# Kernel optimization log

Hardware: AMD Instinct MI355X
Metric: run time of the kernel (lower is better)

Reference implementation:

```python
import jax, jax.numpy as jnp
import numpy as np

EPS = 1e-08


def setup_inputs() -> dict:
    key = jax.random.key(0)
    kx, km = jax.random.split(key)
    B, T, D = 128, 4096, 64
    x = jax.random.normal(kx, (B, T, D), dtype=jnp.float32)
    mask = jax.random.randint(km, (B, T, D), 0, 2).astype(jnp.float32)
    return {"x": x, "mask": mask}


def reference(x, mask):
    B, T, D = x.shape
    dt = x.dtype

    # ---- temporal: lag-1 autocorrelation + linear trend ----
    autocorr = jnp.mean(x[:, :-1, :] * x[:, 1:, :], axis=(1, 2))[:, None]  # (B,1)
    t = jnp.arange(T, dtype=dt)
    t_c = t - t.mean()
    x_mean_t = x.mean(axis=2)                                   # (B,T)
    num = (t_c * (x_mean_t - x_mean_t.mean(axis=1, keepdims=True))).sum(axis=1, keepdims=True)
    trend = num / ((t_c ** 2).sum() + EPS)                      # (B,1)

    # ---- frequency: dominant frequency + spectral entropy ----
    power = jnp.abs(jnp.fft.rfft(x_mean_t, axis=1)) ** 2        # (B,T//2+1)
    dom_freq = (jnp.argmax(power, axis=1).astype(dt) / (T / 2))[:, None]
    p_norm = power / (power.sum(axis=1, keepdims=True) + EPS)
    spec_ent = -(p_norm * jnp.log(p_norm + EPS)).sum(axis=1, keepdims=True)

    # ---- statistical: skewness, kurtosis, quantiles ----
    xc = x - x.mean(axis=(1, 2), keepdims=True)
    m2 = (xc ** 2).mean(axis=(1, 2))
    m3 = (xc ** 3).mean(axis=(1, 2))
    m4 = (xc ** 4).mean(axis=(1, 2))
    skew = m3 / (m2 ** 1.5 + EPS)
    kurt = m4 / (m2 ** 2 + EPS)
    q = jnp.quantile(x.reshape(B, -1), jnp.array([0.25, 0.5, 0.75]), axis=1)  # (3,B)
    stat = jnp.stack([skew, kurt, q[0], q[1], q[2]], axis=1)    # (B,5)

    # ---- shape: peaks, zero crossings, rate of change ----
    diff = x_mean_t[:, 1:] - x_mean_t[:, :-1]                   # (B,T-1)
    peak = (diff[:, 1:] * diff[:, :-1] < 0).astype(dt).sum(axis=1, keepdims=True) / (T - 2)
    xmc = x_mean_t - x_mean_t.mean(axis=1, keepdims=True)
    zero_cross = (xmc[:, 1:] * xmc[:, :-1] < 0).astype(dt).sum(axis=1, keepdims=True) / (T - 1)
    roc = jnp.abs(diff).mean(axis=1, keepdims=True)

    # ---- missing-data features (vectorized, no per-batch loop) ----
    missing_rate = 1.0 - mask.reshape(B, -1).sum(axis=1, keepdims=True) / (T * D + EPS)
    obs_per_time = mask.sum(axis=2)                             # (B,T)
    obs_density = obs_per_time / (D + EPS)
    density_var = jnp.var(obs_density, axis=1, ddof=1, keepdims=True)  # unbiased, matches torch
    time_mask = obs_per_time > 0                                # (B,T) bool
    first_idx = jnp.argmax(time_mask, axis=1).astype(dt)
    first_obs = jnp.where(time_mask.any(axis=1), first_idx / T, 0.0)[:, None]

    # ---- channel features: mean off-diagonal correlation + PCA var explained ----
    xcc = x - x.mean(axis=1, keepdims=True)                     # (B,T,D)
    gram = jnp.einsum('btd,bte->bde', xcc, xcc)                 # (B,D,D)
    cov = gram / (T - 1 + EPS)
    std = jnp.std(x, axis=1, ddof=1)                            # (B,D), unbiased like torch.std
    corr = cov / (std[:, :, None] * std[:, None, :] + EPS)
    off_diag = 1.0 - jnp.eye(D, dtype=dt)
    mean_corr = ((corr * off_diag).sum(axis=(1, 2)) / (D * (D - 1) + EPS))[:, None]
    # singular values squared of xcc == eigenvalues of gram
    eig = jnp.linalg.eigvalsh(gram)                             # ascending, (B,D)
    var_explained = (eig[:, -1] / eig.sum(axis=1))[:, None]

    return jnp.concatenate([
        autocorr, trend,               # temporal (2)
        dom_freq, spec_ent,            # frequency (2)
        stat,                          # statistical (5)
        peak, zero_cross, roc,         # shape (3)
        missing_rate, density_var, first_obs,  # missing (3)
        mean_corr, var_explained,      # channel (2)
    ], axis=1)                          # (B,17)
```

## Files before the change

### kernel.cpp

```cpp
#include <hip/hip_runtime.h>
#include <math.h>

#define TB 128
#define TT 4096
#define TD 64

#define GRAM_OFF   0u
#define HIST_OFF   2097152u
#define COLSUM_OFF 4194304u
#define SCAL_OFF   4227072u
#define FIRST_OFF  4230656u
#define ZERO_BYTES 4231168u
#define XMEAN_OFF  4231168u

typedef float  f32x4  __attribute__((ext_vector_type(4)));
typedef short  s16x8  __attribute__((ext_vector_type(8)));

__device__ __forceinline__ float brs4(float v, float* sbuf, int tid) {
#pragma unroll
  for (int o = 32; o; o >>= 1) v += __shfl_xor(v, o);
  __syncthreads();
  if ((tid & 63) == 0) sbuf[tid >> 6] = v;
  __syncthreads();
  return (sbuf[0] + sbuf[1]) + (sbuf[2] + sbuf[3]);
}

__device__ __forceinline__ float brs8(float v, float* sbuf, int tid) {
#pragma unroll
  for (int o = 32; o; o >>= 1) v += __shfl_xor(v, o);
  __syncthreads();
  if ((tid & 63) == 0) sbuf[tid >> 6] = v;
  __syncthreads();
  return ((sbuf[0] + sbuf[1]) + (sbuf[2] + sbuf[3])) +
         ((sbuf[4] + sbuf[5]) + (sbuf[6] + sbuf[7]));
}

__device__ __forceinline__ int binof(float v) {
  int bi = (int)floorf(fmaf(v, 256.f, 2048.f));
  return bi < 0 ? 0 : (bi > 4095 ? 4095 : bi);
}

__device__ __forceinline__ unsigned short f2bf(float f) {
  unsigned u = __float_as_uint(f);
  return (unsigned short)((u + 0x7FFFu + ((u >> 16) & 1u)) >> 16);
}

__global__ __launch_bounds__(256) void kA_stats(const float* __restrict__ x,
    const float* __restrict__ mk, float* __restrict__ xmean,
    unsigned long long* __restrict__ hist64, float* __restrict__ colsum,
    float* __restrict__ scal, int* __restrict__ firstg) {
  __shared__ unsigned shist[4096];
  __shared__ float xrow[256];
  __shared__ float scol[64];
  __shared__ float sred[4];
  __shared__ int smax[4];

  const int tid  = threadIdx.x;
  const int b    = blockIdx.y;
  const int s    = blockIdx.x;
  const int t0   = s << 8;
  const int lane = tid & 63;
  const int wv   = tid >> 6;
  const int q    = lane >> 4;
  const int c    = lane & 15;
  const int lcol = c << 2;
  const int tw   = t0 + (wv << 6);

  for (int i = tid; i < 4096; i += 256) shist[i] = 0u;
  if (tid < 64) scol[tid] = 0.f;
  __syncthreads();

  float s1 = 0.f, s2 = 0.f, s3 = 0.f, s4 = 0.f, ac = 0.f;
  float osum = 0.f, o2 = 0.f;
  int fmax = 0;
  float cs0 = 0.f, cs1 = 0.f, cs2 = 0.f, cs3 = 0.f;
  float4 pv = make_float4(0.f, 0.f, 0.f, 0.f);

  const float* xb = x + (size_t)b * (TT * TD);
  const float* mb = mk + (size_t)b * (TT * TD);

  for (int it = 0; it < 16; ++it) {
    const int t = tw + (it << 2) + q;
    const float4 v = *(const float4*)(xb + (size_t)t * TD + lcol);
    const float4 m = *(const float4*)(mb + (size_t)t * TD + lcol);
    {
      const float x0 = v.x, x1 = v.y, x2 = v.z, x3 = v.w;
      const float q0 = x0 * x0, q1 = x1 * x1, q2 = x2 * x2, q3 = x3 * x3;
      s1 += (x0 + x1) + (x2 + x3);
      s2 += (q0 + q1) + (q2 + q3);
      s3 += (q0 * x0 + q1 * x1) + (q2 * x2 + q3 * x3);
      s4 += (q0 * q0 + q1 * q1) + (q2 * q2 + q3 * q3);
      cs0 += x0; cs1 += x1; cs2 += x2; cs3 += x3;
      atomicAdd(&shist[binof(x0)], 1u);
      atomicAdd(&shist[binof(x1)], 1u);
      atomicAdd(&shist[binof(x2)], 1u);
      atomicAdd(&shist[binof(x3)], 1u);
    }
    {
      float rx = (v.x + v.y) + (v.z + v.w);
      float rm = (m.x + m.y) + (m.z + m.w);
      rx += __shfl_xor(rx, 1); rm += __shfl_xor(rm, 1);
      rx += __shfl_xor(rx, 2); rm += __shfl_xor(rm, 2);
      rx += __shfl_xor(rx, 4); rm += __shfl_xor(rm, 4);
      rx += __shfl_xor(rx, 8); rm += __shfl_xor(rm, 8);
      if (c == 0) {
        xrow[t - t0] = rx * (1.f / 64.f);
        osum += rm;
        o2 = fmaf(rm, rm, o2);
        if (rm > 0.f) fmax = max(fmax, TT - t);
      }
    }
    {
      const float n0 = __shfl(v.x, lane + 16);
      const float n1 = __shfl(v.y, lane + 16);
      const float n2 = __shfl(v.z, lane + 16);
      const float n3 = __shfl(v.w, lane + 16);
      const float d1 = (v.x * n0 + v.y * n1) + (v.z * n2 + v.w * n3);
      ac += (q < 3) ? d1 : 0.f;
      const float b0 = __shfl(v.x, c);
      const float b1 = __shfl(v.y, c);
      const float b2 = __shfl(v.z, c);
      const float b3 = __shfl(v.w, c);
      if (it > 0) {
        const float d2 = (pv.x * b0 + pv.y * b1) + (pv.z * b2 + pv.w * b3);
        ac += (q == 3) ? d2 : 0.f;
      }
      pv = v;
    }
  }
  {
    const int tnext = tw + 64;
    if (tnext < TT) {
      const float4 nb = *(const float4*)(xb + (size_t)tnext * TD + lcol);
      const float d2 = (pv.x * nb.x + pv.y * nb.y) + (pv.z * nb.z + pv.w * nb.w);
      ac += (q == 3) ? d2 : 0.f;
    }
  }
  __syncthreads();
  xmean[(size_t)b * TT + t0 + tid] = xrow[tid];
  const float rac = brs4(ac, sred, tid);
  const float r1 = brs4(s1, sred, tid);
  const float r2 = brs4(s2, sred, tid);
  const float r3 = brs4(s3, sred, tid);
  const float r4 = brs4(s4, sred, tid);
  const float ro = brs4(osum, sred, tid);
  const float ro2 = brs4(o2, sred, tid);
#pragma unroll
  for (int o = 32; o; o >>= 1) fmax = max(fmax, __shfl_xor(fmax, o));
  if ((tid & 63) == 0) smax[tid >> 6] = fmax;
  __syncthreads();
  if (tid == 0) {
    atomicAdd(&scal[0 * TB + b], rac);
    atomicAdd(&scal[1 * TB + b], r1);
    atomicAdd(&scal[2 * TB + b], r2);
    atomicAdd(&scal[3 * TB + b], r3);
    atomicAdd(&scal[4 * TB + b], r4);
    atomicAdd(&scal[5 * TB + b], ro);
    atomicAdd(&scal[6 * TB + b], ro2);
    atomicMax(&firstg[b], max(max(smax[0], smax[1]), max(smax[2], smax[3])));
  }
  atomicAdd(&scol[lcol + 0], cs0);
  atomicAdd(&scol[lcol + 1], cs1);
  atomicAdd(&scol[lcol + 2], cs2);
  atomicAdd(&scol[lcol + 3], cs3);
  __syncthreads();
  if (tid < 64) atomicAdd(&colsum[b * 64 + tid], scol[tid]);
  unsigned long long* hb = hist64 + (size_t)b * 2048;
  const int rot = (s * 331) & 2047;
  for (int i0 = tid; i0 < 2048; i0 += 256) {
    const int i = (i0 + rot) & 2047;
    const unsigned lo = shist[2 * i];
    const unsigned hi = shist[2 * i + 1];
    if (lo | hi)
      atomicAdd(&hb[i], (unsigned long long)lo | ((unsigned long long)hi << 32));
  }
}

__global__ __launch_bounds__(256) void kB_gram(const float* __restrict__ x,
                                               float* __restrict__ gram) {
  __shared__ __align__(16) unsigned short Xt[2][64 * 72];
  const int tid  = threadIdx.x;
  const int b    = blockIdx.y;
  const int s    = blockIdx.x;
  const int t0   = s << 9;
  const int lane = tid & 63;
  const int wv   = tid >> 6;
  const int g    = tid >> 4;
  const int r0   = g << 2;
  const int c    = tid & 15;
  const int lcol = c << 2;
  const int mb0 = (wv & 1) << 5;
  const int nb0 = (wv >> 1) << 5;
  const int ml  = lane & 15;
  const int qk  = (lane >> 4) << 3;

  f32x4 acc[2][2];
#pragma unroll
  for (int mi = 0; mi < 2; ++mi)
#pragma unroll
    for (int ni = 0; ni < 2; ++ni) acc[mi][ni] = (f32x4)0.f;

  const float* xb = x + (size_t)b * (TT * TD);

  int p = 0;
  for (int tile = 0; tile < 8; ++tile) {
    const int tbase = t0 + (tile << 6);
    float4 v[4];
#pragma unroll
    for (int k = 0; k < 4; ++k)
      v[k] = *(const float4*)(xb + (size_t)(tbase + r0 + k) * TD + lcol);
#pragma unroll
    for (int j = 0; j < 4; ++j) {
      const float e0 = j == 0 ? v[0].x : (j == 1 ? v[0].y : (j == 2 ? v[0].z : v[0].w));
      const float e1 = j == 0 ? v[1].x : (j == 1 ? v[1].y : (j == 2 ? v[1].z : v[1].w));
      const float e2 = j == 0 ? v[2].x : (j == 1 ? v[2].y : (j == 2 ? v[2].z : v[2].w));
      const float e3 = j == 0 ? v[3].x : (j == 1 ? v[3].y : (j == 2 ? v[3].z : v[3].w));
      uint2 pw;
      pw.x = (unsigned)f2bf(e0) | ((unsigned)f2bf(e1) << 16);
      pw.y = (unsigned)f2bf(e2) | ((unsigned)f2bf(e3) << 16);
      *(uint2*)(&Xt[p][(lcol + j) * 72 + r0]) = pw;
    }
    __syncthreads();
#pragma unroll
    for (int kk = 0; kk < 2; ++kk) {
      const int ko = (kk << 5) + qk;
      s16x8 af[2], bf[2];
#pragma unroll
      for (int mi = 0; mi < 2; ++mi)
        af[mi] = *(const s16x8*)(&Xt[p][(mb0 + (mi << 4) + ml) * 72 + ko]);
#pragma unroll
      for (int ni = 0; ni < 2; ++ni)
        bf[ni] = *(const s16x8*)(&Xt[p][(nb0 + (ni << 4) + ml) * 72 + ko]);
#pragma unroll
      for (int mi = 0; mi < 2; ++mi)
#pragma unroll
        for (int ni = 0; ni < 2; ++ni)
          acc[mi][ni] = __builtin_amdgcn_mfma_f32_16x16x32_bf16(
              af[mi], bf[ni], acc[mi][ni], 0, 0, 0);
    }
    p ^= 1;
  }
  float* gb = gram + (size_t)b * 4096;
  const int crow = (lane >> 4) << 2;
  const int ccol = lane & 15;
#pragma unroll
  for (int mi = 0; mi < 2; ++mi)
#pragma unroll
    for (int ni = 0; ni < 2; ++ni) {
      const int gr0 = mb0 + (mi << 4) + crow;
      const int gc = nb0 + (ni << 4) + ccol;
#pragma unroll
      for (int rg = 0; rg < 4; ++rg)
        atomicAdd(&gb[(gr0 + rg) * 64 + gc], acc[mi][ni][rg]);
    }
}

__global__ __launch_bounds__(512) void k34(const float* __restrict__ xmean,
    const float* __restrict__ gram, const float* __restrict__ colsum,
    const unsigned* __restrict__ hist, const float* __restrict__ scal,
    const int* __restrict__ firstg, float* __restrict__ out) {
  __shared__ __align__(16) char arena[49152];
  __shared__ float sred[8];
  __shared__ float smv[8];
  __shared__ int smi[8];
  __shared__ float cssh[64];
  __shared__ float sdsh[64];
  __shared__ float osv_s[6];
  const int tid = threadIdx.x;

  if (blockIdx.x < 128) {
    const int b = blockIdx.x;
    float* xm = (float*)arena;
    float* re = xm + 4096;
    float* im = re + 4096;
    const float* xb = xmean + (size_t)b * TT;
    for (int i = tid; i < TT; i += 512) xm[i] = xb[i];
    __syncthreads();
    float ls = 0.f;
    for (int i = tid; i < TT; i += 512) ls += xm[i];
    const float meanv = brs8(ls, sred, tid) * (1.f / TT);
    float tnum = 0.f, roc = 0.f;
    int pk = 0, zc = 0;
    for (int i = tid; i < TT; i += 512) {
      const float xi = xm[i];
      tnum += ((float)i - 2047.5f) * (xi - meanv);
      if (i < TT - 1) {
        const float d1 = xm[i + 1] - xi;
        roc += fabsf(d1);
        if (i >= 1) {
          const float d0 = xi - xm[i - 1];
          if (d1 * d0 < 0.f) ++pk;
        }
      }
      if (i >= 1) {
        if ((xi - meanv) * (xm[i - 1] - meanv) < 0.f) ++zc;
      }
    }
    tnum = brs8(tnum, sred, tid);
    roc = brs8(roc, sred, tid);
    const float pkf = brs8((float)pk, sred, tid);
    const float zcf = brs8((float)zc, sred, tid);
    if (tid == 0) {
      out[b * 17 + 1] = tnum / 5726622720.0f;
      out[b * 17 + 9] = pkf * (1.f / 4094.f);
      out[b * 17 + 10] = zcf * (1.f / 4095.f);
      out[b * 17 + 11] = roc * (1.f / 4095.f);
    }
    for (int i = tid; i < TT; i += 512) {
      re[i] = xm[__brev((unsigned)i) >> 20];
      im[i] = 0.f;
    }
    __syncthreads();
    int l2h = 0;
    for (int len = 2; len <= TT; len <<= 1, ++l2h) {
      const int half = len >> 1;
      const float ab = -6.283185307179586f / (float)len;
      for (int j = tid; j < TT / 2; j += 512) {
        const int pos = j & (half - 1);
        const int i0 = ((j >> l2h) << (l2h + 1)) + pos;
        const int i1 = i0 + half;
        float sn, cn;
        __sincosf(ab * (float)pos, &sn, &cn);
        const float vr = re[i1], vi = im[i1];
        const float tr = cn * vr - sn * vi;
        const float ti = cn * vi + sn * vr;
        const float ur = re[i0], ui = im[i0];
        re[i0] = ur + tr; im[i0] = ui + ti;
        re[i1] = ur - tr; im[i1] = ui - ti;
      }
      __syncthreads();
    }
    float ps = 0.f, bmaxv = -1.f;
    int bidx = 0;
    for (int k = tid; k <= 2048; k += 512) {
      const float p = re[k] * re[k] + im[k] * im[k];
      ps += p;
      if (p > bmaxv) { bmaxv = p; bidx = k; }
    }
    ps = brs8(ps, sred, tid);
#pragma unroll
    for (int o = 32; o; o >>= 1) {
      const float ov = __shfl_xor(bmaxv, o);
      const int oi = __shfl_xor(bidx, o);
      if (ov > bmaxv || (ov == bmaxv && oi < bidx)) { bmaxv = ov; bidx = oi; }
    }
    if ((tid & 63) == 0) { smv[tid >> 6] = bmaxv; smi[tid >> 6] = bidx; }
    __syncthreads();
    float ent = 0.f;
    const float inv = 1.f / (ps + 1e-8f);
    for (int k = tid; k <= 2048; k += 512) {
      const float p = (re[k] * re[k] + im[k] * im[k]) * inv;
      ent -= p * __logf(p + 1e-8f);
    }
    ent = brs8(ent, sred, tid);
    if (tid == 0) {
      float bv = smv[0]; int bi = smi[0];
      for (int w = 1; w < 8; ++w)
        if (smv[w] > bv || (smv[w] == bv && smi[w] < bi)) { bv = smv[w]; bi = smi[w]; }
      out[b * 17 + 2] = (float)bi * (1.f / 2048.f);
      out[b * 17 + 3] = ent;
    }
  } else {
    const int b = blockIdx.x - 128;
    float* Lg = (float*)arena;
    unsigned* h = (unsigned*)(arena + 16640);
    unsigned* cumc = (unsigned*)(arena + 16640 + 16384);
    if (tid < 64) cssh[tid] = colsum[b * 64 + tid];
    for (int i = tid; i < 4096; i += 512) h[i] = hist[(size_t)b * 4096 + i];
    __syncthreads();
    const float* gb = gram + (size_t)b * 4096;
    for (int i = tid; i < 4096; i += 512) {
      const int d = i >> 6, e = i & 63;
      Lg[d * 65 + e] = gb[i] - cssh[d] * cssh[e] * (1.f / 4096.f);
    }
    unsigned chs_own = 0;
    if (tid < 256) {
#pragma unroll
      for (int j = 0; j < 16; ++j) chs_own += h[(tid << 4) + j];
      cumc[tid] = chs_own;
    }
    __syncthreads();
    if (tid < 64) sdsh[tid] = sqrtf(Lg[tid * 65 + tid] * (1.f / 4095.f));
    for (int off = 1; off < 256; off <<= 1) {
      unsigned add = 0;
      if (tid < 256 && tid >= off) add = cumc[tid - off];
      __syncthreads();
      if (tid < 256) cumc[tid] += add;
      __syncthreads();
    }
    float mcs = 0.f, trc = 0.f;
    for (int i = tid; i < 4096; i += 512) {
      const int d = i >> 6, e = i & 63;
      const float gv = Lg[d * 65 + e];
      if (d != e) mcs += (gv * (1.f / 4095.f)) / (sdsh[d] * sdsh[e] + 1e-8f);
      else trc += gv;
    }
    mcs = brs8(mcs, sred, tid);
    trc = brs8(trc, sred, tid);
    if (tid < 256) {
      const unsigned ranks[6] = {65535u, 65536u, 131071u, 131072u, 196607u, 196608u};
      const unsigned incl = cumc[tid];
      const unsigned excl = incl - chs_own;
#pragma unroll
      for (int qi = 0; qi < 6; ++qi) {
        const unsigned r = ranks[qi];
        if (excl <= r && r < incl) {
          int bin = tid << 4;
          unsigned cum = excl;
          while (bin < 4095 && cum + h[bin] <= r) { cum += h[bin]; ++bin; }
          const float cnt = (float)max(h[bin], 1u);
          osv_s[qi] = ((float)bin * (1.f / 256.f) - 8.f) +
                      (((float)(r - cum) + 0.5f) / cnt) * (1.f / 256.f);
        }
      }
    }
    float lam = 0.f;
    if (tid < 64) {
      const float* rowp = &Lg[tid * 65];
      float v = 1.f + 0.001f * (float)tid;
      float n2 = 1.f;
      for (int it = 0; it < 48; ++it) {
        float w0 = 0.f, w1 = 0.f, w2 = 0.f, w3 = 0.f;
#pragma unroll
        for (int e = 0; e < 64; e += 4) {
          w0 = fmaf(rowp[e],     __shfl(v, e),     w0);
          w1 = fmaf(rowp[e + 1], __shfl(v, e + 1), w1);
          w2 = fmaf(rowp[e + 2], __shfl(v, e + 2), w2);
          w3 = fmaf(rowp[e + 3], __shfl(v, e + 3), w3);
        }
        const float w = (w0 + w1) + (w2 + w3);
        n2 = w * w;
#pragma unroll
        for (int o = 32; o; o >>= 1) n2 += __shfl_xor(n2, o);
        v = w * rsqrtf(n2);
      }
      lam = sqrtf(n2);
    }
    __syncthreads();
    if (tid == 0) {
      const float q25 = 0.25f * osv_s[0] + 0.75f * osv_s[1];
      const float q50 = 0.5f * (osv_s[2] + osv_s[3]);
      const float q75 = 0.75f * osv_s[4] + 0.25f * osv_s[5];
      const float N = 262144.f;
      const float m1 = scal[1 * TB + b] / N;
      const float M2 = scal[2 * TB + b] / N;
      const float M3 = scal[3 * TB + b] / N;
      const float M4 = scal[4 * TB + b] / N;
      const float mu2 = M2 - m1 * m1;
      const float mu3 = M3 - 3.f * m1 * M2 + 2.f * m1 * m1 * m1;
      const float mu4 = M4 - 4.f * m1 * M3 + 6.f * m1 * m1 * M2 - 3.f * m1 * m1 * m1 * m1;
      const float skew = mu3 / (sqrtf(mu2) * mu2 + 1e-8f);
      const float kurt = mu4 / (mu2 * mu2 + 1e-8f);
      const float acv = scal[0 * TB + b] * (1.f / 262080.f);
      const float msum = scal[5 * TB + b];
      const float o2s = scal[6 * TB + b];
      const float missing = 1.f - msum / 262144.f;
      const float sdm = msum * (1.f / 64.f) * (1.f / 4096.f);
      const float dvar = (o2s * (1.f / 4096.f) - 4096.f * sdm * sdm) * (1.f / 4095.f);
      const int fm = firstg[b];
      const float fobs = fm > 0 ? (float)(4096 - fm) * (1.f / 4096.f) : 0.f;
      float* ob = out + b * 17;
      ob[0] = acv;
      ob[4] = skew; ob[5] = kurt;
      ob[6] = q25; ob[7] = q50; ob[8] = q75;
      ob[12] = missing; ob[13] = dvar; ob[14] = fobs;
      ob[15] = mcs / (4032.f + 1e-8f);
      ob[16] = lam / trc;
    }
  }
}

extern "C" void kernel_launch(void* const* d_in, const int* in_sizes, int n_in,
                              void* d_out, int out_size, void* d_ws, size_t ws_size,
                              hipStream_t stream) {
  (void)in_sizes; (void)n_in; (void)out_size; (void)ws_size;
  const float* x = (const float*)d_in[0];
  const float* mask = (const float*)d_in[1];
  float* out = (float*)d_out;
  char* ws = (char*)d_ws;
  float* gram = (float*)(ws + GRAM_OFF);
  unsigned* hist = (unsigned*)(ws + HIST_OFF);
  unsigned long long* hist64 = (unsigned long long*)(ws + HIST_OFF);
  float* colsum = (float*)(ws + COLSUM_OFF);
  float* scal = (float*)(ws + SCAL_OFF);
  int* firstg = (int*)(ws + FIRST_OFF);
  float* xmean = (float*)(ws + XMEAN_OFF);

  hipMemsetAsync(d_ws, 0, ZERO_BYTES, stream);

  dim3 gA(16, TB);
  kA_stats<<<gA, 256, 0, stream>>>(x, mask, xmean, hist64, colsum, scal, firstg);
  dim3 gB(8, TB);
  kB_gram<<<gB, 256, 0, stream>>>(x, gram);
  k34<<<256, 512, 0, stream>>>(xmean, gram, colsum, hist, scal, firstg, out);
}
```

Measured before the change: 358.7 us.

## Process four consecutive rows per thread in stats kernel, halve block count

```diff
diff --git a/kernel.cpp b/kernel.cpp
--- a/kernel.cpp
+++ b/kernel.cpp
@@ -50,7 +50,7 @@
     unsigned long long* __restrict__ hist64, float* __restrict__ colsum,
     float* __restrict__ scal, int* __restrict__ firstg) {
   __shared__ unsigned shist[4096];
-  __shared__ float xrow[256];
+  __shared__ float xrow[512];
   __shared__ float scol[64];
   __shared__ float sred[4];
   __shared__ int smax[4];
@@ -58,13 +58,11 @@
   const int tid  = threadIdx.x;
   const int b    = blockIdx.y;
   const int s    = blockIdx.x;
-  const int t0   = s << 8;
-  const int lane = tid & 63;
-  const int wv   = tid >> 6;
-  const int q    = lane >> 4;
-  const int c    = lane & 15;
+  const int t0   = s << 9;
+  const int g    = tid >> 4;
+  const int r0   = g << 2;
+  const int c    = tid & 15;
   const int lcol = c << 2;
-  const int tw   = t0 + (wv << 6);
 
   for (int i = tid; i < 4096; i += 256) shist[i] = 0u;
   if (tid < 64) scol[tid] = 0.f;
@@ -74,17 +72,25 @@
   float osum = 0.f, o2 = 0.f;
   int fmax = 0;
   float cs0 = 0.f, cs1 = 0.f, cs2 = 0.f, cs3 = 0.f;
-  float4 pv = make_float4(0.f, 0.f, 0.f, 0.f);
 
   const float* xb = x + (size_t)b * (TT * TD);
   const float* mb = mk + (size_t)b * (TT * TD);
 
-  for (int it = 0; it < 16; ++it) {
-    const int t = tw + (it << 2) + q;
-    const float4 v = *(const float4*)(xb + (size_t)t * TD + lcol);
-    const float4 m = *(const float4*)(mb + (size_t)t * TD + lcol);
-    {
-      const float x0 = v.x, x1 = v.y, x2 = v.z, x3 = v.w;
+  for (int tile = 0; tile < 8; ++tile) {
+    const int r = t0 + (tile << 6) + r0;
+    float4 v[4], m[4];
+#pragma unroll
+    for (int k = 0; k < 4; ++k)
+      v[k] = *(const float4*)(xb + (size_t)(r + k) * TD + lcol);
+#pragma unroll
+    for (int k = 0; k < 4; ++k)
+      m[k] = *(const float4*)(mb + (size_t)(r + k) * TD + lcol);
+    float4 nx = make_float4(0.f, 0.f, 0.f, 0.f);
+    if (r + 4 < TT)
+      nx = *(const float4*)(xb + (size_t)(r + 4) * TD + lcol);
+#pragma unroll
+    for (int k = 0; k < 4; ++k) {
+      const float x0 = v[k].x, x1 = v[k].y, x2 = v[k].z, x3 = v[k].w;
       const float q0 = x0 * x0, q1 = x1 * x1, q2 = x2 * x2, q3 = x3 * x3;
       s1 += (x0 + x1) + (x2 + x3);
       s2 += (q0 + q1) + (q2 + q3);
@@ -96,48 +102,30 @@
       atomicAdd(&shist[binof(x2)], 1u);
       atomicAdd(&shist[binof(x3)], 1u);
     }
-    {
-      float rx = (v.x + v.y) + (v.z + v.w);
-      float rm = (m.x + m.y) + (m.z + m.w);
+#pragma unroll
+    for (int k = 0; k < 4; ++k) {
+      float rx = (v[k].x + v[k].y) + (v[k].z + v[k].w);
+      float rm = (m[k].x + m[k].y) + (m[k].z + m[k].w);
       rx += __shfl_xor(rx, 1); rm += __shfl_xor(rm, 1);
       rx += __shfl_xor(rx, 2); rm += __shfl_xor(rm, 2);
       rx += __shfl_xor(rx, 4); rm += __shfl_xor(rm, 4);
       rx += __shfl_xor(rx, 8); rm += __shfl_xor(rm, 8);
       if (c == 0) {
+        const int t = r + k;
         xrow[t - t0] = rx * (1.f / 64.f);
         osum += rm;
         o2 = fmaf(rm, rm, o2);
         if (rm > 0.f) fmax = max(fmax, TT - t);
       }
     }
-    {
-      const float n0 = __shfl(v.x, lane + 16);
-      const float n1 = __shfl(v.y, lane + 16);
-      const float n2 = __shfl(v.z, lane + 16);
-      const float n3 = __shfl(v.w, lane + 16);
-      const float d1 = (v.x * n0 + v.y * n1) + (v.z * n2 + v.w * n3);
-      ac += (q < 3) ? d1 : 0.f;
-      const float b0 = __shfl(v.x, c);
-      const float b1 = __shfl(v.y, c);
-      const float b2 = __shfl(v.z, c);
-      const float b3 = __shfl(v.w, c);
-      if (it > 0) {
-        const float d2 = (pv.x * b0 + pv.y * b1) + (pv.z * b2 + pv.w * b3);
-        ac += (q == 3) ? d2 : 0.f;
-      }
-      pv = v;
-    }
+    ac += (v[0].x * v[1].x + v[0].y * v[1].y) + (v[0].z * v[1].z + v[0].w * v[1].w);
+    ac += (v[1].x * v[2].x + v[1].y * v[2].y) + (v[1].z * v[2].z + v[1].w * v[2].w);
+    ac += (v[2].x * v[3].x + v[2].y * v[3].y) + (v[2].z * v[3].z + v[2].w * v[3].w);
+    ac += (v[3].x * nx.x + v[3].y * nx.y) + (v[3].z * nx.z + v[3].w * nx.w);
   }
-  {
-    const int tnext = tw + 64;
-    if (tnext < TT) {
-      const float4 nb = *(const float4*)(xb + (size_t)tnext * TD + lcol);
-      const float d2 = (pv.x * nb.x + pv.y * nb.y) + (pv.z * nb.z + pv.w * nb.w);
-      ac += (q == 3) ? d2 : 0.f;
-    }
-  }
   __syncthreads();
   xmean[(size_t)b * TT + t0 + tid] = xrow[tid];
+  xmean[(size_t)b * TT + t0 + tid + 256] = xrow[tid + 256];
   const float rac = brs4(ac, sred, tid);
   const float r1 = brs4(s1, sred, tid);
   const float r2 = brs4(s2, sred, tid);
@@ -488,7 +476,7 @@
 
   hipMemsetAsync(d_ws, 0, ZERO_BYTES, stream);
 
-  dim3 gA(16, TB);
+  dim3 gA(8, TB);
   kA_stats<<<gA, 256, 0, stream>>>(x, mask, xmean, hist64, colsum, scal, firstg);
   dim3 gB(8, TB);
   kB_gram<<<gB, 256, 0, stream>>>(x, gram);
```

Result: no change. 355.1 us (-1.0%).
